# Kernel optimization log

Measured on AMD Instinct MI355X. Metric: run time of the kernel, lower is better.

The kernel has to match this reference:

```python
import jax, jax.numpy as jnp
import numpy as np

N, E, F_IN, H, OUT, G = 40000, 640000, 128, 128, 10, 256


def setup_inputs() -> dict:
    key = jax.random.key(0)
    ks = jax.random.split(key, 8)
    x = jax.random.normal(ks[0], (N, F_IN), dtype=jnp.float32)
    edge_index = jax.random.randint(ks[1], (2, E), 0, N, dtype=jnp.int32)
    batch = jnp.sort(jax.random.randint(ks[2], (N,), 0, G, dtype=jnp.int32))
    W1 = jax.random.normal(ks[3], (F_IN, H), dtype=jnp.float32) / np.sqrt(F_IN)
    b1 = jnp.zeros((H,), dtype=jnp.float32)
    W2 = jax.random.normal(ks[4], (H, H), dtype=jnp.float32) / np.sqrt(H)
    b2 = jnp.zeros((H,), dtype=jnp.float32)
    Wfc = jax.random.normal(ks[5], (H, OUT), dtype=jnp.float32) / np.sqrt(H)
    bfc = jnp.zeros((OUT,), dtype=jnp.float32)
    return {"x": x, "edge_index": edge_index, "batch": batch,
            "W1": W1, "b1": b1, "W2": W2, "b2": b2, "Wfc": Wfc, "bfc": bfc}


def _gcn_conv(x, W, b, row, col, num_nodes):
    # x' = D^{-1/2} (A+I) D^{-1/2} (x W) + b   (self-loops already in row/col)
    xw = x @ W                                            # [N, H]
    ones = jnp.ones(row.shape[0], dtype=x.dtype)
    deg = jax.ops.segment_sum(ones, col, num_segments=num_nodes)
    dinv = jnp.where(deg > 0, jax.lax.rsqrt(jnp.maximum(deg, 1.0)), 0.0)
    norm = dinv[row] * dinv[col]                          # [E+N]
    msg = xw[row] * norm[:, None]                         # gather + scale
    return jax.ops.segment_sum(msg, col, num_segments=num_nodes) + b


def reference(x, edge_index, batch, W1, b1, W2, b2, Wfc, bfc):
    num_nodes = x.shape[0]
    loop = jnp.arange(num_nodes, dtype=edge_index.dtype)
    row = jnp.concatenate([edge_index[0], loop])
    col = jnp.concatenate([edge_index[1], loop])

    h = jax.nn.relu(_gcn_conv(x, W1, b1, row, col, num_nodes))
    h = jax.nn.relu(_gcn_conv(h, W2, b2, row, col, num_nodes))

    # global_mean_pool over graph ids
    sums = jax.ops.segment_sum(h, batch, num_segments=G)  # [G, H]
    cnt = jax.ops.segment_sum(jnp.ones(num_nodes, h.dtype), batch, num_segments=G)
    pooled = sums / jnp.maximum(cnt, 1.0)[:, None]

    logits = pooled @ Wfc + bfc                           # [G, OUT]
    return jax.nn.log_softmax(logits, axis=-1)
```

## Files before the change

### kernel.cpp

```cpp
#include <hip/hip_runtime.h>
#include <hip/hip_fp16.h>
#include <math.h>

#define H_DIM 128
#define OUT_DIM 10

typedef __attribute__((ext_vector_type(8))) __bf16 bf16x8;
typedef __attribute__((ext_vector_type(8))) unsigned short ushort8;
typedef __attribute__((ext_vector_type(4))) float f32x4;

__device__ inline unsigned short f2bf_rne(float f) {
    unsigned int u = __float_as_uint(f);
    unsigned int r = u + 0x7FFFu + ((u >> 16) & 1u);
    return (unsigned short)(r >> 16);
}
__device__ inline float bf_lo(unsigned int u) { return __uint_as_float(u << 16); }
__device__ inline float bf_hi(unsigned int u) { return __uint_as_float(u & 0xFFFF0000u); }
__device__ inline float h2f(unsigned int e) {
    return __half2float(__ushort_as_half((unsigned short)(e & 0xFFFFu)));
}

#define ACC4(gv, nv) do { \
    const unsigned int* _u = (const unsigned int*)&(gv); \
    ax[0] += bf_lo(_u[0]) * (nv); ay[0] += bf_hi(_u[0]) * (nv); \
    ax[1] += bf_lo(_u[1]) * (nv); ay[1] += bf_hi(_u[1]) * (nv); \
    ax[2] += bf_lo(_u[2]) * (nv); ay[2] += bf_hi(_u[2]) * (nv); \
    ax[3] += bf_lo(_u[3]) * (nv); ay[3] += bf_hi(_u[3]) * (nv); \
} while (0)

#define SEG_BODY(ce, m) do { \
    int groups = ((m) + 3) >> 2; \
    int g = 0; \
    for (; g + 3 < groups; g += 4) { \
        int j = g * 4 + sub; \
        unsigned int e0 = __shfl((int)(ce), j); \
        unsigned int e1 = __shfl((int)(ce), j + 4); \
        unsigned int e2 = __shfl((int)(ce), j + 8); \
        unsigned int e3 = __shfl((int)(ce), j + 12); \
        int4 g0 = XW16[(size_t)(e0 >> 16) * 16 + fl]; \
        int4 g1 = XW16[(size_t)(e1 >> 16) * 16 + fl]; \
        int4 g2 = XW16[(size_t)(e2 >> 16) * 16 + fl]; \
        int4 g3 = XW16[(size_t)(e3 >> 16) * 16 + fl]; \
        float n0 = h2f(e0), n1 = h2f(e1), n2 = h2f(e2), n3 = h2f(e3); \
        ACC4(g0, n0); ACC4(g1, n1); ACC4(g2, n2); ACC4(g3, n3); \
    } \
    for (; g < groups; ++g) { \
        int j = g * 4 + sub; \
        unsigned int e = __shfl((int)(ce), j); \
        int4 gg = XW16[(size_t)(e >> 16) * 16 + fl]; \
        float n = h2f(e); \
        ACC4(gg, n); \
    } \
} while (0)

__device__ inline void gather_node_pre(const int4* __restrict__ XW16,
                                       const unsigned int* __restrict__ csr,
                                       int start, int end, int c, float dc2,
                                       unsigned int ce0, int4 gs,
                                       int sub, int fl, int lane,
                                       float ax[4], float ay[4]) {
    {
        float s = (sub == 0) ? dc2 : 0.0f;
        const unsigned int* u = (const unsigned int*)&gs;
        ax[0] = bf_lo(u[0]) * s; ay[0] = bf_hi(u[0]) * s;
        ax[1] = bf_lo(u[1]) * s; ay[1] = bf_hi(u[1]) * s;
        ax[2] = bf_lo(u[2]) * s; ay[2] = bf_hi(u[2]) * s;
        ax[3] = bf_lo(u[3]) * s; ay[3] = bf_hi(u[3]) * s;
    }
    int m0 = end - start; if (m0 > 64) m0 = 64;
    SEG_BODY(ce0, m0);
    for (int base = start + 64; base < end; base += 64) {
        int m = end - base; if (m > 64) m = 64;
        unsigned int ce = ((unsigned int)c) << 16;
        if (lane < m) ce = csr[base + lane];
        SEG_BODY(ce, m);
    }
    #pragma unroll
    for (int q = 0; q < 4; ++q) {
        ax[q] += __shfl_xor(ax[q], 16); ax[q] += __shfl_xor(ax[q], 32);
        ay[q] += __shfl_xor(ay[q], 16); ay[q] += __shfl_xor(ay[q], 32);
    }
}

__device__ inline void gather_node(const int4* __restrict__ XW16,
                                   const unsigned int* __restrict__ csr,
                                   int start, int end, int c, float dc2,
                                   int sub, int fl, int lane,
                                   float ax[4], float ay[4]) {
    int m0 = end - start; if (m0 > 64) m0 = 64;
    unsigned int ce0 = ((unsigned int)c) << 16;
    if (lane < m0) ce0 = csr[start + lane];
    int4 gs = XW16[(size_t)c * 16 + fl];
    gather_node_pre(XW16, csr, start, end, c, dc2, ce0, gs, sub, fl, lane, ax, ay);
}

__global__ __launch_bounds__(256) void prep_kernel(const float* __restrict__ W1,
                                                   const float* __restrict__ W2,
                                                   unsigned short* __restrict__ Wt1Hi,
                                                   unsigned short* __restrict__ Wt1Lo,
                                                   unsigned short* __restrict__ Wt2Hi,
                                                   unsigned short* __restrict__ Wt2Lo,
                                                   int hb,
                                                   const int* __restrict__ col,
                                                   int* __restrict__ cnt,
                                                   int* __restrict__ rank, int E) {
    if (blockIdx.x < (unsigned)hb) {
        int e = blockIdx.x * 256 + threadIdx.x;
        if (e < E) rank[e] = atomicAdd(&cnt[col[e]], 1);
    } else {
        int i = (blockIdx.x - hb) * 256 + threadIdx.x;
        const float* src   = (i < 16384) ? W1    : W2;
        unsigned short* dh = (i < 16384) ? Wt1Hi : Wt2Hi;
        unsigned short* dl = (i < 16384) ? Wt1Lo : Wt2Lo;
        int idx = i & 16383;
        int k = idx >> 7, n = idx & 127;
        float v = src[idx];
        unsigned short hbv = f2bf_rne(v);
        float hf = __uint_as_float((unsigned int)hbv << 16);
        unsigned short lb = f2bf_rne(v - hf);
        dh[n * H_DIM + k] = hbv;
        dl[n * H_DIM + k] = lb;
    }
}

__global__ __launch_bounds__(256) void scan_phase1(const int* __restrict__ cnt,
                                                   int* __restrict__ blockSums,
                                                   float* __restrict__ dinv, int N) {
    __shared__ int red[256];
    int base = blockIdx.x * 1024;
    int t = threadIdx.x;
    int s = 0;
    for (int i = 0; i < 4; ++i) {
        int idx = base + t * 4 + i;
        if (idx < N) {
            int cv = cnt[idx];
            s += cv;
            dinv[idx] = rsqrtf((float)cv + 1.0f);
        }
    }
    red[t] = s;
    __syncthreads();
    for (int d = 128; d > 0; d >>= 1) {
        if (t < d) red[t] += red[t + d];
        __syncthreads();
    }
    if (t == 0) blockSums[blockIdx.x] = red[0];
}

__global__ __launch_bounds__(256) void scan_phase23(const int* __restrict__ cnt,
                                                    const int* __restrict__ blockSums,
                                                    int* __restrict__ offs, int N, int B) {
    __shared__ int red[256];
    __shared__ int bsum[256];
    int base = blockIdx.x * 1024;
    int t = threadIdx.x;

    bsum[t] = (t < B && t < (int)blockIdx.x) ? blockSums[t] : 0;

    int v[4];
    int s = 0;
    for (int i = 0; i < 4; ++i) {
        int idx = base + t * 4 + i;
        v[i] = (idx < N) ? cnt[idx] : 0;
        s += v[i];
    }
    red[t] = s;
    __syncthreads();
    for (int d = 128; d > 0; d >>= 1) {
        if (t < d) bsum[t] += bsum[t + d];
        __syncthreads();
    }
    for (int d = 1; d < 256; d <<= 1) {
        int x = (t >= d) ? red[t - d] : 0;
        __syncthreads();
        red[t] += x;
        __syncthreads();
    }
    int run = bsum[0] + ((t == 0) ? 0 : red[t - 1]);
    for (int i = 0; i < 4; ++i) {
        int idx = base + t * 4 + i;
        if (idx < N) { offs[idx] = run; run += v[i]; }
    }
    if ((int)blockIdx.x == B - 1 && t == 255) offs[N] = run;
}

__global__ __launch_bounds__(256) void scatter_gemm1(
        const int* __restrict__ row, const int* __restrict__ col,
        const int* __restrict__ rank, const float* __restrict__ dinv,
        const int* __restrict__ offs, unsigned int* __restrict__ csr, int E, int sb,
        const float* __restrict__ Xf,
        const unsigned short* __restrict__ WtHi, const unsigned short* __restrict__ WtLo,
        unsigned short* __restrict__ Yb, int N) {
    if (blockIdx.x < (unsigned)sb) {
        int e = blockIdx.x * 256 + threadIdx.x;
        if (e >= E) return;
        int r = row[e], c = col[e], rk = rank[e];
        int pos = offs[c] + rk;
        float norm = dinv[r] * dinv[c];
        unsigned short nb = __half_as_ushort(__float2half(norm));
        csr[pos] = (((unsigned int)r) << 16) | nb;
        return;
    }
    int blk  = blockIdx.x - sb;
    int lane = threadIdx.x & 63;
    int wv   = threadIdx.x >> 6;
    int m16  = lane & 15;
    int quad = lane >> 4;
    int nodeBase = blk * 32;

    f32x4 acc[2][2] = {};

    #pragma unroll
    for (int kt = 0; kt < 4; ++kt) {
        int k0 = kt * 32 + quad * 8;

        ushort8 aHi[2], aLo[2];
        #pragma unroll
        for (int mi = 0; mi < 2; ++mi) {
            int node = nodeBase + mi * 16 + m16;
            if (node >= N) node = N - 1;
            const float* p = Xf + (size_t)node * H_DIM + k0;
            f32x4 u = *(const f32x4*)p;
            f32x4 w = *(const f32x4*)(p + 4);
            float vv[8] = {u.x, u.y, u.z, u.w, w.x, w.y, w.z, w.w};
            #pragma unroll
            for (int j = 0; j < 8; ++j) {
                unsigned short hbv = f2bf_rne(vv[j]);
                aHi[mi][j] = hbv;
                aLo[mi][j] = f2bf_rne(vv[j] - __uint_as_float((unsigned int)hbv << 16));
            }
        }

        ushort8 bHi[2], bLo[2];
        #pragma unroll
        for (int ni = 0; ni < 2; ++ni) {
            int n = (wv * 2 + ni) * 16 + m16;
            size_t off = (size_t)n * H_DIM + k0;
            bHi[ni] = *(const ushort8*)(WtHi + off);
            bLo[ni] = *(const ushort8*)(WtLo + off);
        }

        #pragma unroll
        for (int mi = 0; mi < 2; ++mi)
            #pragma unroll
            for (int ni = 0; ni < 2; ++ni) {
                acc[mi][ni] = __builtin_amdgcn_mfma_f32_16x16x32_bf16(
                    __builtin_bit_cast(bf16x8, aHi[mi]),
                    __builtin_bit_cast(bf16x8, bHi[ni]), acc[mi][ni], 0, 0, 0);
                acc[mi][ni] = __builtin_amdgcn_mfma_f32_16x16x32_bf16(
                    __builtin_bit_cast(bf16x8, aLo[mi]),
                    __builtin_bit_cast(bf16x8, bHi[ni]), acc[mi][ni], 0, 0, 0);
                acc[mi][ni] = __builtin_amdgcn_mfma_f32_16x16x32_bf16(
                    __builtin_bit_cast(bf16x8, aHi[mi]),
                    __builtin_bit_cast(bf16x8, bLo[ni]), acc[mi][ni], 0, 0, 0);
            }
    }

    #pragma unroll
    for (int mi = 0; mi < 2; ++mi)
        #pragma unroll
        for (int r = 0; r < 4; ++r) {
            int node = nodeBase + mi * 16 + quad * 4 + r;
            if (node < N) {
                #pragma unroll
                for (int ni = 0; ni < 2; ++ni) {
                    int c = (wv * 2 + ni) * 16 + m16;
                    Yb[(size_t)node * H_DIM + c] = f2bf_rne(acc[mi][ni][r]);
                }
            }
        }
}

__global__ __launch_bounds__(256) void agg1_gemm2(
        const unsigned short* __restrict__ XWb,
        const float* __restrict__ dinv,
        const unsigned int* __restrict__ csr,
        const int* __restrict__ offs,
        const float* __restrict__ bias,
        const unsigned short* __restrict__ WtHi,
        const unsigned short* __restrict__ WtLo,
        unsigned short* __restrict__ Yb,
        int N) {
    __shared__ __align__(16) unsigned short hrow[16][136];
    int lane = threadIdx.x & 63;
    int wv   = threadIdx.x >> 6;
    int sub  = lane >> 4;
    int fl   = lane & 15;
    int nodeBase = blockIdx.x * 16;
    const int4* XW16 = (const int4*)XWb;
    float4 b0 = ((const float4*)bias)[fl * 2];
    float4 b1 = ((const float4*)bias)[fl * 2 + 1];

    int cN[4], st[4], en[4];
    float dc2[4];
    #pragma unroll
    for (int i = 0; i < 4; ++i) {
        int c = nodeBase + wv * 4 + i;
        bool ok = c < N;
        int cc = ok ? c : N - 1;
        cN[i] = cc;
        st[i] = ok ? offs[cc] : 0;
        en[i] = ok ? offs[cc + 1] : 0;
        float d = dinv[cc];
        dc2[i] = ok ? d * d : 0.f;
    }
    unsigned int ce0[4]; int4 gs[4];
    #pragma unroll
    for (int i = 0; i < 4; ++i) {
        int m = en[i] - st[i]; if (m > 64) m = 64;
        unsigned int pad = ((unsigned int)cN[i]) << 16;
        ce0[i] = (lane < m) ? csr[st[i] + lane] : pad;
        gs[i] = XW16[(size_t)cN[i] * 16 + fl];
    }

    #pragma unroll
    for (int i = 0; i < 4; ++i) {
        float ax[4], ay[4];
        gather_node_pre(XW16, csr, st[i], en[i], cN[i], dc2[i],
                        ce0[i], gs[i], sub, fl, lane, ax, ay);
        ax[0] = fmaxf(ax[0] + b0.x, 0.f); ay[0] = fmaxf(ay[0] + b0.y, 0.f);
        ax[1] = fmaxf(ax[1] + b0.z, 0.f); ay[1] = fmaxf(ay[1] + b0.w, 0.f);
        ax[2] = fmaxf(ax[2] + b1.x, 0.f); ay[2] = fmaxf(ay[2] + b1.y, 0.f);
        ax[3] = fmaxf(ax[3] + b1.z, 0.f); ay[3] = fmaxf(ay[3] + b1.w, 0.f);
        if (sub == 0) {
            unsigned int o[4];
            #pragma unroll
            for (int q = 0; q < 4; ++q)
                o[q] = (unsigned int)f2bf_rne(ax[q]) | ((unsigned int)f2bf_rne(ay[q]) << 16);
            *(int4*)&hrow[wv * 4 + i][fl * 8] = *(const int4*)o;
        }
    }
    __syncthreads();

    int m16  = lane & 15;
    int quad = lane >> 4;
    f32x4 acc[2] = {};
    #pragma unroll
    for (int kt = 0; kt < 4; ++kt) {
        int k0 = kt * 32 + quad * 8;
        ushort8 a = *(const ushort8*)&hrow[m16][k0];
        #pragma unroll
        for (int ni = 0; ni < 2; ++ni) {
            int n = (wv * 2 + ni) * 16 + m16;
            size_t off = (size_t)n * H_DIM + k0;
            ushort8 bHi = *(const ushort8*)(WtHi + off);
            ushort8 bLo = *(const ushort8*)(WtLo + off);
            acc[ni] = __builtin_amdgcn_mfma_f32_16x16x32_bf16(
                __builtin_bit_cast(bf16x8, a),
                __builtin_bit_cast(bf16x8, bHi), acc[ni], 0, 0, 0);
            acc[ni] = __builtin_amdgcn_mfma_f32_16x16x32_bf16(
                __builtin_bit_cast(bf16x8, a),
                __builtin_bit_cast(bf16x8, bLo), acc[ni], 0, 0, 0);
        }
    }
    #pragma unroll
    for (int r = 0; r < 4; ++r) {
        int node = nodeBase + quad * 4 + r;
        if (node < N) {
            #pragma unroll
            for (int ni = 0; ni < 2; ++ni) {
                int cc = (wv * 2 + ni) * 16 + m16;
                Yb[(size_t)node * H_DIM + cc] = f2bf_rne(acc[ni][r]);
            }
        }
    }
}

__global__ __launch_bounds__(256) void agg_pool(const unsigned short* __restrict__ XWb,
                                                const float* __restrict__ dinv,
                                                const unsigned int* __restrict__ csr,
                                                const int* __restrict__ offs,
                                                const float* __restrict__ bias,
                                                const int* __restrict__ batch,
                                                float* __restrict__ pooledSum, int N) {
    int wave = (blockIdx.x * 256 + threadIdx.x) >> 6;
    int lane = threadIdx.x & 63;
    int wv   = threadIdx.x >> 6;
    int sub  = lane >> 4;
    int fl   = lane & 15;
    bool active = wave < N;

    float ax[4] = {}, ay[4] = {};
    int c = wave;
    if (active) {
        int start = offs[c], end = offs[c + 1];
        float dc = dinv[c];
        gather_node((const int4*)XWb, csr, start, end, c, dc * dc, sub, fl, lane, ax, ay);
        float4 b0 = ((const float4*)bias)[fl * 2];
        float4 b1 = ((const float4*)bias)[fl * 2 + 1];
        ax[0] = fmaxf(ax[0] + b0.x, 0.f); ay[0] = fmaxf(ay[0] + b0.y, 0.f);
        ax[1] = fmaxf(ax[1] + b0.z, 0.f); ay[1] = fmaxf(ay[1] + b0.w, 0.f);
        ax[2] = fmaxf(ax[2] + b1.x, 0.f); ay[2] = fmaxf(ay[2] + b1.y, 0.f);
        ax[3] = fmaxf(ax[3] + b1.z, 0.f); ay[3] = fmaxf(ay[3] + b1.w, 0.f);
    }

    __shared__ float lacc[4][H_DIM];
    __shared__ int lg[4];
    if (lane == 0) lg[wv] = active ? batch[c] : -1;
    if (sub == 0) {
        float4 f0; f0.x = ax[0]; f0.y = ay[0]; f0.z = ax[1]; f0.w = ay[1];
        float4 f1; f1.x = ax[2]; f1.y = ay[2]; f1.z = ax[3]; f1.w = ay[3];
        ((float4*)&lacc[wv][fl * 8])[0] = f0;
        ((float4*)&lacc[wv][fl * 8])[1] = f1;
    }
    __syncthreads();
    int t = threadIdx.x;
    if (t < H_DIM) {
        float s = 0.f; int cur = -1;
        #pragma unroll
        for (int w = 0; w < 4; ++w) {
            int g = lg[w];
            if (g < 0) continue;
            if (g != cur) {
                if (cur >= 0) atomicAdd(&pooledSum[cur * H_DIM + t], s);
                s = 0.f; cur = g;
            }
            s += lacc[w][t];
        }
        if (cur >= 0) atomicAdd(&pooledSum[cur * H_DIM + t], s);
    }
}

__global__ __launch_bounds__(64) void head_kernel(const float* __restrict__ pooledSum,
                                                  const int* __restrict__ batch,
                                                  const float* __restrict__ Wfc,
                                                  const float* __restrict__ bfc,
                                                  float* __restrict__ out, int N) {
    __shared__ float sl[OUT_DIM + 2];
    __shared__ int bounds[2];
    int g = blockIdx.x;
    int j = threadIdx.x;
    if (j < 2) {
        int v = g + j;
        int lo = 0, hi = N;
        while (lo < hi) {
            int mid = (lo + hi) >> 1;
            if (batch[mid] < v) lo = mid + 1; else hi = mid;
        }
        bounds[j] = lo;
    }
    __syncthreads();
    int cnt = bounds[1] - bounds[0];
    float inv = 1.0f / (float)(cnt > 0 ? cnt : 1);
    if (j < OUT_DIM) {
        float acc = 0.f;
        const float* p = pooledSum + g * H_DIM;
        for (int k = 0; k < H_DIM; ++k) acc += p[k] * Wfc[k * OUT_DIM + j];
        sl[j] = acc * inv + bfc[j];
    }
    __syncthreads();
    if (j == 0) {
        float m = sl[0];
        for (int i = 1; i < OUT_DIM; ++i) m = fmaxf(m, sl[i]);
        float s = 0.f;
        for (int i = 0; i < OUT_DIM; ++i) s += expf(sl[i] - m);
        sl[OUT_DIM] = m + logf(s);
    }
    __syncthreads();
    if (j < OUT_DIM) out[g * OUT_DIM + j] = sl[j] - sl[OUT_DIM];
}

extern "C" void kernel_launch(void* const* d_in, const int* in_sizes, int n_in,
                              void* d_out, int out_size, void* d_ws, size_t ws_size,
                              hipStream_t stream) {
    const float* x     = (const float*)d_in[0];
    const int*   ei    = (const int*)  d_in[1];
    const int*   batch = (const int*)  d_in[2];
    const float* W1    = (const float*)d_in[3];
    const float* b1    = (const float*)d_in[4];
    const float* W2    = (const float*)d_in[5];
    const float* b2    = (const float*)d_in[6];
    const float* Wfc   = (const float*)d_in[7];
    const float* bfc   = (const float*)d_in[8];
    float* out = (float*)d_out;

    int N = in_sizes[2];
    int E = in_sizes[1] / 2;
    int G = out_size / OUT_DIM;
    const int* row = ei;
    const int* col = ei + E;

    char* wsb = (char*)d_ws;
    size_t nAlign = (size_t)((N + 256) / 256) * 256;
    size_t eAlign = (size_t)((E + 255) / 256) * 256;
    int*   cnt       = (int*)wsb;
    float* pooledSum = (float*)(cnt + nAlign);
    int*   offs      = (int*)(pooledSum + (size_t)G * H_DIM);
    int*   rank      = offs + nAlign;
    float* dinv      = (float*)(rank + eAlign);
    unsigned int* csr = (unsigned int*)(dinv + nAlign);
    unsigned short* Xb = (unsigned short*)(csr + eAlign);
    unsigned short* Hb = Xb + (size_t)N * H_DIM;
    int* blockSums = (int*)(Hb + (size_t)N * H_DIM);
    unsigned short* Wt1Hi = (unsigned short*)(blockSums + 256);
    unsigned short* Wt1Lo = Wt1Hi + H_DIM * H_DIM;
    unsigned short* Wt2Hi = Wt1Lo + H_DIM * H_DIM;
    unsigned short* Wt2Lo = Wt2Hi + H_DIM * H_DIM;

    int scanBlocks = (N + 1023) / 1024;
    int histBlocks = (E + 255) / 256;
    int gemmBlocks = (N + 31) / 32;

    hipMemsetAsync(cnt, 0, (nAlign + (size_t)G * H_DIM) * sizeof(int), stream);

    prep_kernel<<<histBlocks + 128, 256, 0, stream>>>(
        W1, W2, Wt1Hi, Wt1Lo, Wt2Hi, Wt2Lo, histBlocks, col, cnt, rank, E);

    scan_phase1<<<scanBlocks, 256, 0, stream>>>(cnt, blockSums, dinv, N);
    scan_phase23<<<scanBlocks, 256, 0, stream>>>(cnt, blockSums, offs, N, scanBlocks);

    scatter_gemm1<<<histBlocks + gemmBlocks, 256, 0, stream>>>(
        row, col, rank, dinv, offs, csr, E, histBlocks,
        x, Wt1Hi, Wt1Lo, Xb, N);

    int ag1Blocks = (N + 15) / 16;
    agg1_gemm2<<<ag1Blocks, 256, 0, stream>>>(Xb, dinv, csr, offs, b1,
                                              Wt2Hi, Wt2Lo, Hb, N);

    int aggBlocks = (N + 3) / 4;
    agg_pool<<<aggBlocks, 256, 0, stream>>>(Hb, dinv, csr, offs, b2,
                                            batch, pooledSum, N);

    head_kernel<<<G, 64, 0, stream>>>(pooledSum, batch, Wfc, bfc, out, N);
}
```

Before: 224.1 us.

## Replace stored per-edge rank with second atomic counter and drop gather prefetch

The histogram pass no longer stores a per-edge rank array. The CSR scatter now takes each edge's slot from a second zeroed counter array via atomicAdd, which removes the rank write and read traffic but adds a second round of atomics. The agg1 kernel also drops its batched prefetch of the first CSR chunk and self row for its four nodes and processes nodes sequentially with a merged gather_node. This simplifies the code but gives up memory-level parallelism in that kernel. CSR order within a segment becomes nondeterministic, which changes float summation order.

```diff
diff --git a/kernel.cpp b/kernel.cpp
--- a/kernel.cpp
+++ b/kernel.cpp
@@ -53,23 +53,21 @@
     } \
 } while (0)
 
-__device__ inline void gather_node_pre(const int4* __restrict__ XW16,
-                                       const unsigned int* __restrict__ csr,
-                                       int start, int end, int c, float dc2,
-                                       unsigned int ce0, int4 gs,
-                                       int sub, int fl, int lane,
-                                       float ax[4], float ay[4]) {
+__device__ inline void gather_node(const int4* __restrict__ XW16,
+                                   const unsigned int* __restrict__ csr,
+                                   int start, int end, int c, float dc2,
+                                   int sub, int fl, int lane,
+                                   float ax[4], float ay[4]) {
     {
         float s = (sub == 0) ? dc2 : 0.0f;
+        int4 gs = XW16[(size_t)c * 16 + fl];
         const unsigned int* u = (const unsigned int*)&gs;
         ax[0] = bf_lo(u[0]) * s; ay[0] = bf_hi(u[0]) * s;
         ax[1] = bf_lo(u[1]) * s; ay[1] = bf_hi(u[1]) * s;
         ax[2] = bf_lo(u[2]) * s; ay[2] = bf_hi(u[2]) * s;
         ax[3] = bf_lo(u[3]) * s; ay[3] = bf_hi(u[3]) * s;
     }
-    int m0 = end - start; if (m0 > 64) m0 = 64;
-    SEG_BODY(ce0, m0);
-    for (int base = start + 64; base < end; base += 64) {
+    for (int base = start; base < end; base += 64) {
         int m = end - base; if (m > 64) m = 64;
         unsigned int ce = ((unsigned int)c) << 16;
         if (lane < m) ce = csr[base + lane];
@@ -80,18 +78,6 @@
         ax[q] += __shfl_xor(ax[q], 16); ax[q] += __shfl_xor(ax[q], 32);
         ay[q] += __shfl_xor(ay[q], 16); ay[q] += __shfl_xor(ay[q], 32);
     }
-}
-
-__device__ inline void gather_node(const int4* __restrict__ XW16,
-                                   const unsigned int* __restrict__ csr,
-                                   int start, int end, int c, float dc2,
-                                   int sub, int fl, int lane,
-                                   float ax[4], float ay[4]) {
-    int m0 = end - start; if (m0 > 64) m0 = 64;
-    unsigned int ce0 = ((unsigned int)c) << 16;
-    if (lane < m0) ce0 = csr[start + lane];
-    int4 gs = XW16[(size_t)c * 16 + fl];
-    gather_node_pre(XW16, csr, start, end, c, dc2, ce0, gs, sub, fl, lane, ax, ay);
 }
 
 __global__ __launch_bounds__(256) void prep_kernel(const float* __restrict__ W1,
@@ -102,11 +88,10 @@
                                                    unsigned short* __restrict__ Wt2Lo,
                                                    int hb,
                                                    const int* __restrict__ col,
-                                                   int* __restrict__ cnt,
-                                                   int* __restrict__ rank, int E) {
+                                                   int* __restrict__ cnt, int E) {
     if (blockIdx.x < (unsigned)hb) {
         int e = blockIdx.x * 256 + threadIdx.x;
-        if (e < E) rank[e] = atomicAdd(&cnt[col[e]], 1);
+        if (e < E) atomicAdd(&cnt[col[e]], 1);
     } else {
         int i = (blockIdx.x - hb) * 256 + threadIdx.x;
         const float* src   = (i < 16384) ? W1    : W2;
@@ -186,7 +171,7 @@
 
 __global__ __launch_bounds__(256) void scatter_gemm1(
         const int* __restrict__ row, const int* __restrict__ col,
-        const int* __restrict__ rank, const float* __restrict__ dinv,
+        int* __restrict__ cnt2, const float* __restrict__ dinv,
         const int* __restrict__ offs, unsigned int* __restrict__ csr, int E, int sb,
         const float* __restrict__ Xf,
         const unsigned short* __restrict__ WtHi, const unsigned short* __restrict__ WtLo,
@@ -194,9 +179,10 @@
     if (blockIdx.x < (unsigned)sb) {
         int e = blockIdx.x * 256 + threadIdx.x;
         if (e >= E) return;
-        int r = row[e], c = col[e], rk = rank[e];
+        int r = row[e], c = col[e];
+        float norm = dinv[r] * dinv[c];
+        int rk = atomicAdd(&cnt2[c], 1);
         int pos = offs[c] + rk;
-        float norm = dinv[r] * dinv[c];
         unsigned short nb = __half_as_ushort(__float2half(norm));
         csr[pos] = (((unsigned int)r) << 16) | nb;
         return;
@@ -291,37 +277,18 @@
     float4 b0 = ((const float4*)bias)[fl * 2];
     float4 b1 = ((const float4*)bias)[fl * 2 + 1];
 
-    int cN[4], st[4], en[4];
-    float dc2[4];
-    #pragma unroll
     for (int i = 0; i < 4; ++i) {
         int c = nodeBase + wv * 4 + i;
-        bool ok = c < N;
-        int cc = ok ? c : N - 1;
-        cN[i] = cc;
-        st[i] = ok ? offs[cc] : 0;
-        en[i] = ok ? offs[cc + 1] : 0;
-        float d = dinv[cc];
-        dc2[i] = ok ? d * d : 0.f;
-    }
-    unsigned int ce0[4]; int4 gs[4];
-    #pragma unroll
-    for (int i = 0; i < 4; ++i) {
-        int m = en[i] - st[i]; if (m > 64) m = 64;
-        unsigned int pad = ((unsigned int)cN[i]) << 16;
-        ce0[i] = (lane < m) ? csr[st[i] + lane] : pad;
-        gs[i] = XW16[(size_t)cN[i] * 16 + fl];
-    }
-
-    #pragma unroll
-    for (int i = 0; i < 4; ++i) {
-        float ax[4], ay[4];
-        gather_node_pre(XW16, csr, st[i], en[i], cN[i], dc2[i],
-                        ce0[i], gs[i], sub, fl, lane, ax, ay);
-        ax[0] = fmaxf(ax[0] + b0.x, 0.f); ay[0] = fmaxf(ay[0] + b0.y, 0.f);
-        ax[1] = fmaxf(ax[1] + b0.z, 0.f); ay[1] = fmaxf(ay[1] + b0.w, 0.f);
-        ax[2] = fmaxf(ax[2] + b1.x, 0.f); ay[2] = fmaxf(ay[2] + b1.y, 0.f);
-        ax[3] = fmaxf(ax[3] + b1.z, 0.f); ay[3] = fmaxf(ay[3] + b1.w, 0.f);
+        float ax[4] = {}, ay[4] = {};
+        if (c < N) {
+            int start = offs[c], end = offs[c + 1];
+            float dc = dinv[c];
+            gather_node(XW16, csr, start, end, c, dc * dc, sub, fl, lane, ax, ay);
+            ax[0] = fmaxf(ax[0] + b0.x, 0.f); ay[0] = fmaxf(ay[0] + b0.y, 0.f);
+            ax[1] = fmaxf(ax[1] + b0.z, 0.f); ay[1] = fmaxf(ay[1] + b0.w, 0.f);
+            ax[2] = fmaxf(ax[2] + b1.x, 0.f); ay[2] = fmaxf(ay[2] + b1.y, 0.f);
+            ax[3] = fmaxf(ax[3] + b1.z, 0.f); ay[3] = fmaxf(ay[3] + b1.w, 0.f);
+        }
         if (sub == 0) {
             unsigned int o[4];
             #pragma unroll
@@ -485,9 +452,9 @@
     size_t eAlign = (size_t)((E + 255) / 256) * 256;
     int*   cnt       = (int*)wsb;
     float* pooledSum = (float*)(cnt + nAlign);
-    int*   offs      = (int*)(pooledSum + (size_t)G * H_DIM);
-    int*   rank      = offs + nAlign;
-    float* dinv      = (float*)(rank + eAlign);
+    int*   cnt2      = (int*)(pooledSum + (size_t)G * H_DIM);
+    int*   offs      = cnt2 + nAlign;
+    float* dinv      = (float*)(offs + nAlign);
     unsigned int* csr = (unsigned int*)(dinv + nAlign);
     unsigned short* Xb = (unsigned short*)(csr + eAlign);
     unsigned short* Hb = Xb + (size_t)N * H_DIM;
@@ -501,16 +468,16 @@
     int histBlocks = (E + 255) / 256;
     int gemmBlocks = (N + 31) / 32;
 
-    hipMemsetAsync(cnt, 0, (nAlign + (size_t)G * H_DIM) * sizeof(int), stream);
+    hipMemsetAsync(cnt, 0, (nAlign + (size_t)G * H_DIM + nAlign) * sizeof(int), stream);
 
     prep_kernel<<<histBlocks + 128, 256, 0, stream>>>(
-        W1, W2, Wt1Hi, Wt1Lo, Wt2Hi, Wt2Lo, histBlocks, col, cnt, rank, E);
+        W1, W2, Wt1Hi, Wt1Lo, Wt2Hi, Wt2Lo, histBlocks, col, cnt, E);
 
     scan_phase1<<<scanBlocks, 256, 0, stream>>>(cnt, blockSums, dinv, N);
     scan_phase23<<<scanBlocks, 256, 0, stream>>>(cnt, blockSums, offs, N, scanBlocks);
 
     scatter_gemm1<<<histBlocks + gemmBlocks, 256, 0, stream>>>(
-        row, col, rank, dinv, offs, csr, E, histBlocks,
+        row, col, cnt2, dinv, offs, csr, E, histBlocks,
         x, Wt1Hi, Wt1Lo, Xb, N);
 
     int ag1Blocks = (N + 15) / 16;
```

Result: slower. 240.1 us (+7.1%).
